# Performance work log

Hardware: AMD Instinct MI355X
Metric: run time of the kernel (lower is better)

Reference implementation:

```python
import jax, jax.numpy as jnp
import numpy as np

H = 100          # hidden size (hard-coded in module)
B, C, T = 256, 9, 1024
NC = 6           # num_classes


def _lstm_layer(xs, W_ih, W_hh, b, h0, c0):
    """xs: [B,T,In] -> hidden sequence [B,T,H]. Torch gate order i,f,g,o."""
    # Precompute the input projection for all timesteps in one big GEMM.
    pre = jnp.einsum('bti,gi->btg', xs, W_ih) + b   # [B,T,4H]
    pre_t = jnp.swapaxes(pre, 0, 1)                 # [T,B,4H]

    def step(carry, p):
        h, c = carry
        g = p + h @ W_hh.T                          # [B,4H]
        i, f, gg, o = jnp.split(g, 4, axis=-1)
        c = jax.nn.sigmoid(f) * c + jax.nn.sigmoid(i) * jnp.tanh(gg)
        h = jax.nn.sigmoid(o) * jnp.tanh(c)
        return (h, c), h

    (_, _), hs = jax.lax.scan(step, (h0, c0), pre_t)
    return jnp.swapaxes(hs, 0, 1)                   # [B,T,H]


def setup_inputs() -> dict:
    key = jax.random.key(0)
    ks = jax.random.split(key, 14)
    s = 0.1  # ~ uniform(-1/sqrt(H), 1/sqrt(H)) scale of torch default init
    n = lambda k, shape, sc=s: jax.random.normal(k, shape, dtype=jnp.float32) * sc
    return {
        'x':     jax.random.normal(ks[0], (B, C, T), dtype=jnp.float32),
        'h0_1':  jax.random.normal(ks[1], (B, H), dtype=jnp.float32),
        'c0_1':  jax.random.normal(ks[2], (B, H), dtype=jnp.float32),
        'h0_2':  jax.random.normal(ks[3], (B, H), dtype=jnp.float32),
        'c0_2':  jax.random.normal(ks[4], (B, H), dtype=jnp.float32),
        'W_ih1': n(ks[5], (4 * H, C)),
        'W_hh1': n(ks[6], (4 * H, H)),
        'b1':    n(ks[7], (4 * H,)),   # b_ih + b_hh folded together
        'W_ih2': n(ks[8], (4 * H, H)),
        'W_hh2': n(ks[9], (4 * H, H)),
        'b2':    n(ks[10], (4 * H,)),
        'W_fc':  n(ks[11], (NC, H)),
        'b_fc':  n(ks[12], (NC,)),
    }


def reference(x, h0_1, c0_1, h0_2, c0_2, W_ih1, W_hh1, b1,
              W_ih2, W_hh2, b2, W_fc, b_fc):
    xs = jnp.swapaxes(x, 1, 2)                      # [B,T,C] (x.transpose(1,2))
    h1 = _lstm_layer(xs, W_ih1, W_hh1, b1, h0_1, c0_1)   # [B,T,H]
    h2 = _lstm_layer(h1, W_ih2, W_hh2, b2, h0_2, c0_2)   # [B,T,H]
    out = h2[:, -1, :] @ W_fc.T + b_fc              # [B,NC]
    return out
```

## Files before the change

### kernel.cpp

```cpp
#include <hip/hip_runtime.h>

#define HH   100
#define G4   400
#define BB   256
#define CC   9
#define TT   1024
#define NCLS 6
#define XSTR 13
#define CH   64
#define NCH  (TT/CH)
#define TSTR 128

__device__ __forceinline__ float sigm(float x) {
    return __fdividef(1.0f, 1.0f + __expf(-x));
}
__device__ __forceinline__ float tanh_fast(float x) {
    return 2.0f * sigm(2.0f * x) - 1.0f;
}
__device__ __forceinline__ float bcast(float v, int l) {
    return __int_as_float(__builtin_amdgcn_readlane(__float_as_int(v), l));
}

__global__ __launch_bounds__(512, 2)
void lstm_layer1(const float* __restrict__ x,
                 const float* __restrict__ h0,
                 const float* __restrict__ c0,
                 const float* __restrict__ W_ih,
                 const float* __restrict__ W_hh,
                 const float* __restrict__ bias_g,
                 float* __restrict__ h1out)
{
    const int b    = blockIdx.x;
    const int tid  = threadIdx.x;
    const int lane = tid & 63;

    __shared__ float xT[TT * XSTR + 64];
    __shared__ float hb[128];
    __shared__ float gates[448];

    const float* xb = x + (size_t)b * CC * TT;
    for (int i = tid; i < CC * TT; i += 512) {
        int c  = i >> 10;
        int tp = i & 1023;
        xT[tp * XSTR + c] = xb[i];
    }
    if (tid < 128) hb[tid] = (tid < HH) ? h0[b * HH + tid] : 0.0f;
    float c_reg = (tid < HH) ? c0[b * HH + tid] : 0.0f;

    const bool comp = (tid < 448);
    const int  row  = (tid < G4) ? tid : 0;

    float w[CC + HH], bg = 0.0f;
    if (comp) {
        #pragma unroll
        for (int j = 0; j < CC; ++j) w[j] = W_ih[row * CC + j];
        #pragma unroll
        for (int j = 0; j < HH; ++j) w[CC + j] = W_hh[row * HH + j];
        bg = bias_g[row];
        #pragma unroll
        for (int j = 0; j < CC + HH; ++j) asm volatile("" : "+v"(w[j]));
    }
    const bool isG = (row >= 2 * HH && row < 3 * HH);
    float* hout = h1out + (size_t)b * TT * HH;
    __syncthreads();

    #pragma unroll 1
    for (int t = 0; t < TT; ++t) {
        if (comp) {
            float vx = xT[t * XSTR + lane];
            float va = hb[lane];
            float vb = hb[64 + lane];
            asm volatile("" : "+v"(vx), "+v"(va), "+v"(vb));
            float a0 = bg, a1 = 0.f;
            #pragma unroll
            for (int c = 0; c < CC; ++c) {
                float h_ = bcast(vx, c);
                if (c & 1) a1 += h_ * w[c]; else a0 += h_ * w[c];
            }
            #pragma unroll
            for (int j = 0; j < 64; ++j) {
                float h_ = bcast(va, j);
                if (j & 1) a1 += h_ * w[CC + j]; else a0 += h_ * w[CC + j];
            }
            #pragma unroll
            for (int j = 0; j < 36; ++j) {
                float h_ = bcast(vb, j);
                if (j & 1) a1 += h_ * w[CC + 64 + j]; else a0 += h_ * w[CC + 64 + j];
            }
            gates[tid] = a0 + a1;
        }
        __syncthreads();
        if (tid < HH) {
            float ri = gates[tid];
            float rf = gates[tid + HH];
            float rg = gates[tid + 2 * HH];
            float ro = gates[tid + 3 * HH];
            float cc = sigm(rf) * c_reg + sigm(ri) * tanh_fast(rg);
            c_reg = cc;
            float hv = sigm(ro) * tanh_fast(cc);
            hb[tid] = hv;
            hout[t * HH + tid] = hv;
        }
        __syncthreads();
    }
    (void)isG;
}

__global__ __launch_bounds__(512, 2)
void lstm_layer2_fc(const float* __restrict__ h1,
                    const float* __restrict__ h0,
                    const float* __restrict__ c0,
                    const float* __restrict__ W_ih,
                    const float* __restrict__ W_hh,
                    const float* __restrict__ bias_g,
                    const float* __restrict__ W_fc,
                    const float* __restrict__ b_fc,
                    float* __restrict__ out)
{
    const int b    = blockIdx.x;
    const int tid  = threadIdx.x;
    const int lane = tid & 63;

    __shared__ float tile[CH * TSTR];
    __shared__ float preS[CH * G4];
    __shared__ float hb[128];

    if (tid < 128) hb[tid] = (tid < HH) ? h0[b * HH + tid] : 0.0f;
    float c_reg = (tid < HH) ? c0[b * HH + tid] : 0.0f;

    const bool comp = (tid < 448);
    const int  row  = (tid < G4) ? tid : 0;
    const float bg  = comp ? bias_g[row] : 0.0f;

    const float* h1b = h1 + (size_t)b * TT * HH;
    __syncthreads();

    #pragma unroll 1
    for (int ch = 0; ch < NCH; ++ch) {
        const int t0 = ch * CH;
        for (int i = tid; i < CH * 25; i += 512) {
            int r = i / 25;
            int c = i - r * 25;
            ((float4*)(tile + r * TSTR))[c] =
                ((const float4*)(h1b + (size_t)(t0 + r) * HH))[c];
        }
        __syncthreads();

        {
            const float* wsrc = W_ih + (size_t)row * HH;
            asm volatile("" : "+v"(wsrc));
            if (comp) {
                float wv[HH];
                #pragma unroll
                for (int j = 0; j < HH / 4; ++j)
                    *(float4*)&wv[4 * j] = ((const float4*)wsrc)[j];
                #pragma unroll
                for (int j = 0; j < HH; ++j) asm volatile("" : "+v"(wv[j]));
                #pragma unroll 1
                for (int t = 0; t < CH; ++t) {
                    float va = tile[t * TSTR + lane];
                    float vb = tile[t * TSTR + 64 + lane];
                    asm volatile("" : "+v"(va), "+v"(vb));
                    float a0 = bg, a1 = 0.f;
                    #pragma unroll
                    for (int j = 0; j < 64; ++j) {
                        float h_ = bcast(va, j);
                        if (j & 1) a1 += h_ * wv[j]; else a0 += h_ * wv[j];
                    }
                    #pragma unroll
                    for (int j = 0; j < 36; ++j) {
                        float h_ = bcast(vb, j);
                        if (j & 1) a1 += h_ * wv[64 + j]; else a0 += h_ * wv[64 + j];
                    }
                    if (tid < G4) preS[t * G4 + row] = a0 + a1;
                }
            }
        }
        __syncthreads();

        {
            const float* wsrc = W_hh + (size_t)row * HH;
            asm volatile("" : "+v"(wsrc));
            float wv[HH];
            if (comp) {
                #pragma unroll
                for (int j = 0; j < HH / 4; ++j)
                    *(float4*)&wv[4 * j] = ((const float4*)wsrc)[j];
                #pragma unroll
                for (int j = 0; j < HH; ++j) asm volatile("" : "+v"(wv[j]));
            }
            #pragma unroll 1
            for (int t = 0; t < CH; ++t) {
                if (comp) {
                    float va = hb[lane];
                    float vb = hb[64 + lane];
                    asm volatile("" : "+v"(va), "+v"(vb));
                    float a0 = 0.f, a1 = 0.f;
                    #pragma unroll
                    for (int j = 0; j < 64; ++j) {
                        float h_ = bcast(va, j);
                        if (j & 1) a1 += h_ * wv[j]; else a0 += h_ * wv[j];
                    }
                    #pragma unroll
                    for (int j = 0; j < 36; ++j) {
                        float h_ = bcast(vb, j);
                        if (j & 1) a1 += h_ * wv[64 + j]; else a0 += h_ * wv[64 + j];
                    }
                    if (tid < G4) preS[t * G4 + row] += a0 + a1;
                }
                __syncthreads();
                if (tid < HH) {
                    float ri = preS[t * G4 + tid];
                    float rf = preS[t * G4 + HH + tid];
                    float rg = preS[t * G4 + 2 * HH + tid];
                    float ro = preS[t * G4 + 3 * HH + tid];
                    float cc = sigm(rf) * c_reg + sigm(ri) * tanh_fast(rg);
                    c_reg = cc;
                    hb[tid] = sigm(ro) * tanh_fast(cc);
                }
                __syncthreads();
            }
        }
    }

    if (tid < NCLS) {
        float acc = b_fc[tid];
        #pragma unroll 4
        for (int j = 0; j < HH; ++j) acc += W_fc[tid * HH + j] * hb[j];
        out[b * NCLS + tid] = acc;
    }
}

extern "C" void kernel_launch(void* const* d_in, const int* in_sizes, int n_in,
                              void* d_out, int out_size, void* d_ws, size_t ws_size,
                              hipStream_t stream) {
    const float* x     = (const float*)d_in[0];
    const float* h0_1  = (const float*)d_in[1];
    const float* c0_1  = (const float*)d_in[2];
    const float* h0_2  = (const float*)d_in[3];
    const float* c0_2  = (const float*)d_in[4];
    const float* W_ih1 = (const float*)d_in[5];
    const float* W_hh1 = (const float*)d_in[6];
    const float* b1    = (const float*)d_in[7];
    const float* W_ih2 = (const float*)d_in[8];
    const float* W_hh2 = (const float*)d_in[9];
    const float* b2    = (const float*)d_in[10];
    const float* W_fc  = (const float*)d_in[11];
    const float* b_fc  = (const float*)d_in[12];
    float* out = (float*)d_out;

    float* h1 = (float*)d_ws;

    lstm_layer1<<<BB, 512, 0, stream>>>(x, h0_1, c0_1, W_ih1, W_hh1, b1, h1);
    lstm_layer2_fc<<<BB, 512, 0, stream>>>(h1, h0_2, c0_2, W_ih2, W_hh2, b2,
                                           W_fc, b_fc, out);
}
```

Before: 2.926 ms.

## Split input projections into parallel kernels and chunk recurrence across launches

Moves the input-projection GEMMs for both LSTM layers out of the serial recurrence into separate xproj/hproj kernels that run over a 2D grid of batch by time tile. A shared lstm_rec kernel then runs only the h·W_hh recurrence over time chunks, reading precomputed gates from a workspace buffer and carrying h/c state between launches. The goal is to take the parallel input-projection work off the latency-bound sequential path of layer 2. The cost is more kernel launches, extra global-memory traffic for the pre-activation buffer, and a dependence on workspace size for the chunk length.

```diff
diff --git a/kernel.cpp b/kernel.cpp
--- a/kernel.cpp
+++ b/kernel.cpp
@@ -6,10 +6,6 @@
 #define CC   9
 #define TT   1024
 #define NCLS 6
-#define XSTR 13
-#define CH   64
-#define NCH  (TT/CH)
-#define TSTR 128
 
 __device__ __forceinline__ float sigm(float x) {
     return __fdividef(1.0f, 1.0f + __expf(-x));
@@ -20,74 +16,160 @@
 __device__ __forceinline__ float bcast(float v, int l) {
     return __int_as_float(__builtin_amdgcn_readlane(__float_as_int(v), l));
 }
+__device__ __forceinline__ const float* launder(const float* p) {
+    asm volatile("" : "+v"(p));
+    return p;
+}
 
 __global__ __launch_bounds__(512, 2)
-void lstm_layer1(const float* __restrict__ x,
-                 const float* __restrict__ h0,
-                 const float* __restrict__ c0,
-                 const float* __restrict__ W_ih,
-                 const float* __restrict__ W_hh,
-                 const float* __restrict__ bias_g,
-                 float* __restrict__ h1out)
+void xproj(const float* __restrict__ x,
+           const float* __restrict__ W_ih,
+           const float* __restrict__ bias,
+           float* __restrict__ pre,
+           int tbase, int chSteps)
+{
+    const int b    = blockIdx.x;
+    const int tile = blockIdx.y;
+    const int tid  = threadIdx.x;
+    const int t0g  = tbase + tile * 64;
+
+    __shared__ float xt[CC][64];
+    for (int i = tid; i < CC * 64; i += 512) {
+        int c = i >> 6, k = i & 63;
+        xt[c][k] = x[(size_t)b * CC * TT + c * TT + t0g + k];
+    }
+    __syncthreads();
+
+    if (tid < G4) {
+        const float* w = launder(W_ih + tid * CC);
+        float wv[CC];
+        #pragma unroll
+        for (int c = 0; c < CC; ++c) wv[c] = w[c];
+        const float bg = bias[tid];
+        float* po = pre + ((size_t)b * chSteps + tile * 64) * G4 + tid;
+        #pragma unroll 1
+        for (int k = 0; k < 64; ++k) {
+            float a = bg;
+            #pragma unroll
+            for (int c = 0; c < CC; ++c) a += wv[c] * xt[c][k];
+            po[(size_t)k * G4] = a;
+        }
+    }
+}
+
+__global__ __launch_bounds__(512, 2)
+void hproj(const float* __restrict__ h1,
+           const float* __restrict__ W_ih,
+           const float* __restrict__ bias,
+           float* __restrict__ pre,
+           int tbase, int chSteps)
+{
+    const int b    = blockIdx.x;
+    const int tile = blockIdx.y;
+    const int tid  = threadIdx.x;
+    const int lane = tid & 63;
+    const int t0g  = tbase + tile * 64;
+
+    __shared__ float ht[64][128];
+    for (int i = tid; i < 64 * 25; i += 512) {
+        int r = i / 25, c = i - r * 25;
+        *((float4*)&ht[r][4 * c]) =
+            *((const float4*)(h1 + ((size_t)b * TT + t0g + r) * HH) + c);
+    }
+    __syncthreads();
+
+    if (tid < 448) {
+        const int row = (tid < G4) ? tid : 0;
+        const float* w = launder(W_ih + row * HH);
+        float wv[HH];
+        #pragma unroll
+        for (int j = 0; j < HH / 4; ++j)
+            *(float4*)&wv[4 * j] = ((const float4*)w)[j];
+        const float bg = bias[row];
+        float* po = pre + ((size_t)b * chSteps + tile * 64) * G4 + row;
+        #pragma unroll 1
+        for (int k = 0; k < 64; ++k) {
+            float va = ht[k][lane];
+            float vb = ht[k][64 + lane];
+            asm volatile("" : "+v"(va), "+v"(vb));
+            float a0 = bg, a1 = 0.f;
+            #pragma unroll
+            for (int j = 0; j < 64; ++j) {
+                float s = bcast(va, j);
+                if (j & 1) a1 += s * wv[j]; else a0 += s * wv[j];
+            }
+            #pragma unroll
+            for (int j = 0; j < 36; ++j) {
+                float s = bcast(vb, j);
+                if (j & 1) a1 += s * wv[64 + j]; else a0 += s * wv[64 + j];
+            }
+            if (tid < G4) po[(size_t)k * G4] = a0 + a1;
+        }
+    }
+}
+
+__global__ __launch_bounds__(512, 2)
+void lstm_rec(const float* __restrict__ pre,
+              const float* __restrict__ h0,
+              const float* __restrict__ c0,
+              const float* __restrict__ W_hh,
+              float* __restrict__ h1out,
+              float* __restrict__ st,
+              const float* __restrict__ W_fc,
+              const float* __restrict__ b_fc,
+              float* __restrict__ out,
+              int tbase, int chSteps, int flags)
 {
     const int b    = blockIdx.x;
     const int tid  = threadIdx.x;
     const int lane = tid & 63;
-
-    __shared__ float xT[TT * XSTR + 64];
+    const bool first = (tbase == 0);
+
     __shared__ float hb[128];
     __shared__ float gates[448];
 
-    const float* xb = x + (size_t)b * CC * TT;
-    for (int i = tid; i < CC * TT; i += 512) {
-        int c  = i >> 10;
-        int tp = i & 1023;
-        xT[tp * XSTR + c] = xb[i];
-    }
-    if (tid < 128) hb[tid] = (tid < HH) ? h0[b * HH + tid] : 0.0f;
-    float c_reg = (tid < HH) ? c0[b * HH + tid] : 0.0f;
+    if (tid < 128)
+        hb[tid] = (tid < HH)
+                    ? (first ? h0[b * HH + tid] : st[b * 200 + tid])
+                    : 0.0f;
+    float c_reg = (tid < HH)
+                    ? (first ? c0[b * HH + tid] : st[b * 200 + HH + tid])
+                    : 0.0f;
 
     const bool comp = (tid < 448);
     const int  row  = (tid < G4) ? tid : 0;
-
-    float w[CC + HH], bg = 0.0f;
+    float wv[HH];
     if (comp) {
+        const float* w = launder(W_hh + row * HH);
         #pragma unroll
-        for (int j = 0; j < CC; ++j) w[j] = W_ih[row * CC + j];
-        #pragma unroll
-        for (int j = 0; j < HH; ++j) w[CC + j] = W_hh[row * HH + j];
-        bg = bias_g[row];
-        #pragma unroll
-        for (int j = 0; j < CC + HH; ++j) asm volatile("" : "+v"(w[j]));
-    }
-    const bool isG = (row >= 2 * HH && row < 3 * HH);
-    float* hout = h1out + (size_t)b * TT * HH;
+        for (int j = 0; j < HH / 4; ++j)
+            *(float4*)&wv[4 * j] = ((const float4*)w)[j];
+    }
+    const float* pb = pre + (size_t)b * chSteps * G4;
+    float preg = comp ? pb[row] : 0.0f;
+    float* hout = (flags & 1) ? (h1out + ((size_t)b * TT + tbase) * HH) : nullptr;
     __syncthreads();
 
     #pragma unroll 1
-    for (int t = 0; t < TT; ++t) {
+    for (int t = 0; t < chSteps; ++t) {
         if (comp) {
-            float vx = xT[t * XSTR + lane];
+            float pnext = (t + 1 < chSteps) ? pb[(size_t)(t + 1) * G4 + row] : 0.f;
             float va = hb[lane];
             float vb = hb[64 + lane];
-            asm volatile("" : "+v"(vx), "+v"(va), "+v"(vb));
-            float a0 = bg, a1 = 0.f;
-            #pragma unroll
-            for (int c = 0; c < CC; ++c) {
-                float h_ = bcast(vx, c);
-                if (c & 1) a1 += h_ * w[c]; else a0 += h_ * w[c];
-            }
+            asm volatile("" : "+v"(va), "+v"(vb));
+            float a0 = preg, a1 = 0.f;
             #pragma unroll
             for (int j = 0; j < 64; ++j) {
-                float h_ = bcast(va, j);
-                if (j & 1) a1 += h_ * w[CC + j]; else a0 += h_ * w[CC + j];
+                float s = bcast(va, j);
+                if (j & 1) a1 += s * wv[j]; else a0 += s * wv[j];
             }
             #pragma unroll
             for (int j = 0; j < 36; ++j) {
-                float h_ = bcast(vb, j);
-                if (j & 1) a1 += h_ * w[CC + 64 + j]; else a0 += h_ * w[CC + 64 + j];
+                float s = bcast(vb, j);
+                if (j & 1) a1 += s * wv[64 + j]; else a0 += s * wv[64 + j];
             }
             gates[tid] = a0 + a1;
+            preg = pnext;
         }
         __syncthreads();
         if (tid < HH) {
@@ -99,131 +181,16 @@
             c_reg = cc;
             float hv = sigm(ro) * tanh_fast(cc);
             hb[tid] = hv;
-            hout[t * HH + tid] = hv;
+            if (flags & 1) hout[(size_t)t * HH + tid] = hv;
         }
         __syncthreads();
     }
-    (void)isG;
-}
-
-__global__ __launch_bounds__(512, 2)
-void lstm_layer2_fc(const float* __restrict__ h1,
-                    const float* __restrict__ h0,
-                    const float* __restrict__ c0,
-                    const float* __restrict__ W_ih,
-                    const float* __restrict__ W_hh,
-                    const float* __restrict__ bias_g,
-                    const float* __restrict__ W_fc,
-                    const float* __restrict__ b_fc,
-                    float* __restrict__ out)
-{
-    const int b    = blockIdx.x;
-    const int tid  = threadIdx.x;
-    const int lane = tid & 63;
-
-    __shared__ float tile[CH * TSTR];
-    __shared__ float preS[CH * G4];
-    __shared__ float hb[128];
-
-    if (tid < 128) hb[tid] = (tid < HH) ? h0[b * HH + tid] : 0.0f;
-    float c_reg = (tid < HH) ? c0[b * HH + tid] : 0.0f;
-
-    const bool comp = (tid < 448);
-    const int  row  = (tid < G4) ? tid : 0;
-    const float bg  = comp ? bias_g[row] : 0.0f;
-
-    const float* h1b = h1 + (size_t)b * TT * HH;
-    __syncthreads();
-
-    #pragma unroll 1
-    for (int ch = 0; ch < NCH; ++ch) {
-        const int t0 = ch * CH;
-        for (int i = tid; i < CH * 25; i += 512) {
-            int r = i / 25;
-            int c = i - r * 25;
-            ((float4*)(tile + r * TSTR))[c] =
-                ((const float4*)(h1b + (size_t)(t0 + r) * HH))[c];
-        }
-        __syncthreads();
-
-        {
-            const float* wsrc = W_ih + (size_t)row * HH;
-            asm volatile("" : "+v"(wsrc));
-            if (comp) {
-                float wv[HH];
-                #pragma unroll
-                for (int j = 0; j < HH / 4; ++j)
-                    *(float4*)&wv[4 * j] = ((const float4*)wsrc)[j];
-                #pragma unroll
-                for (int j = 0; j < HH; ++j) asm volatile("" : "+v"(wv[j]));
-                #pragma unroll 1
-                for (int t = 0; t < CH; ++t) {
-                    float va = tile[t * TSTR + lane];
-                    float vb = tile[t * TSTR + 64 + lane];
-                    asm volatile("" : "+v"(va), "+v"(vb));
-                    float a0 = bg, a1 = 0.f;
-                    #pragma unroll
-                    for (int j = 0; j < 64; ++j) {
-                        float h_ = bcast(va, j);
-                        if (j & 1) a1 += h_ * wv[j]; else a0 += h_ * wv[j];
-                    }
-                    #pragma unroll
-                    for (int j = 0; j < 36; ++j) {
-                        float h_ = bcast(vb, j);
-                        if (j & 1) a1 += h_ * wv[64 + j]; else a0 += h_ * wv[64 + j];
-                    }
-                    if (tid < G4) preS[t * G4 + row] = a0 + a1;
-                }
-            }
-        }
-        __syncthreads();
-
-        {
-            const float* wsrc = W_hh + (size_t)row * HH;
-            asm volatile("" : "+v"(wsrc));
-            float wv[HH];
-            if (comp) {
-                #pragma unroll
-                for (int j = 0; j < HH / 4; ++j)
-                    *(float4*)&wv[4 * j] = ((const float4*)wsrc)[j];
-                #pragma unroll
-                for (int j = 0; j < HH; ++j) asm volatile("" : "+v"(wv[j]));
-            }
-            #pragma unroll 1
-            for (int t = 0; t < CH; ++t) {
-                if (comp) {
-                    float va = hb[lane];
-                    float vb = hb[64 + lane];
-                    asm volatile("" : "+v"(va), "+v"(vb));
-                    float a0 = 0.f, a1 = 0.f;
-                    #pragma unroll
-                    for (int j = 0; j < 64; ++j) {
-                        float h_ = bcast(va, j);
-                        if (j & 1) a1 += h_ * wv[j]; else a0 += h_ * wv[j];
-                    }
-                    #pragma unroll
-                    for (int j = 0; j < 36; ++j) {
-                        float h_ = bcast(vb, j);
-                        if (j & 1) a1 += h_ * wv[64 + j]; else a0 += h_ * wv[64 + j];
-                    }
-                    if (tid < G4) preS[t * G4 + row] += a0 + a1;
-                }
-                __syncthreads();
-                if (tid < HH) {
-                    float ri = preS[t * G4 + tid];
-                    float rf = preS[t * G4 + HH + tid];
-                    float rg = preS[t * G4 + 2 * HH + tid];
-                    float ro = preS[t * G4 + 3 * HH + tid];
-                    float cc = sigm(rf) * c_reg + sigm(ri) * tanh_fast(rg);
-                    c_reg = cc;
-                    hb[tid] = sigm(ro) * tanh_fast(cc);
-                }
-                __syncthreads();
-            }
-        }
-    }
-
-    if (tid < NCLS) {
+
+    if (tid < HH) {
+        st[b * 200 + tid]      = hb[tid];
+        st[b * 200 + HH + tid] = c_reg;
+    }
+    if ((flags & 2) && tid < NCLS) {
         float acc = b_fc[tid];
         #pragma unroll 4
         for (int j = 0; j < HH; ++j) acc += W_fc[tid * HH + j] * hb[j];
@@ -249,9 +216,33 @@
     const float* b_fc  = (const float*)d_in[12];
     float* out = (float*)d_out;
 
-    float* h1 = (float*)d_ws;
-
-    lstm_layer1<<<BB, 512, 0, stream>>>(x, h0_1, c0_1, W_ih1, W_hh1, b1, h1);
-    lstm_layer2_fc<<<BB, 512, 0, stream>>>(h1, h0_2, c0_2, W_ih2, W_hh2, b2,
-                                           W_fc, b_fc, out);
-}
+    char* ws = (char*)d_ws;
+    const size_t h1_bytes = (size_t)BB * TT * HH * 4;
+    const size_t st_bytes = (size_t)BB * 200 * 4;
+    float* h1  = (float*)ws;
+    float* st1 = (float*)(ws + h1_bytes);
+    float* st2 = (float*)(ws + h1_bytes + st_bytes);
+    float* pre = (float*)(ws + h1_bytes + 2 * st_bytes);
+
+    size_t avail = (ws_size > h1_bytes + 2 * st_bytes)
+                     ? ws_size - h1_bytes - 2 * st_bytes : 0;
+    int CH = (int)(avail / ((size_t)BB * G4 * 4));
+    CH = (CH / 64) * 64;
+    if (CH > TT) CH = TT;
+    if (CH < 64) CH = 64;
+    if (CH > 256) CH = 256;
+
+    for (int t0 = 0; t0 < TT; t0 += CH) {
+        int ns = (TT - t0 < CH) ? (TT - t0) : CH;
+        xproj<<<dim3(BB, ns / 64), 512, 0, stream>>>(x, W_ih1, b1, pre, t0, ns);
+        lstm_rec<<<BB, 512, 0, stream>>>(pre, h0_1, c0_1, W_hh1, h1, st1,
+                                         nullptr, nullptr, nullptr, t0, ns, 1);
+    }
+    for (int t0 = 0; t0 < TT; t0 += CH) {
+        int ns = (TT - t0 < CH) ? (TT - t0) : CH;
+        int flags = (t0 + ns >= TT) ? 2 : 0;
+        hproj<<<dim3(BB, ns / 64), 512, 0, stream>>>(h1, W_ih2, b2, pre, t0, ns);
+        lstm_rec<<<BB, 512, 0, stream>>>(pre, h0_2, c0_2, W_hh2, nullptr, st2,
+                                         W_fc, b_fc, out, t0, ns, flags);
+    }
+}
```

Result: no change. 2.929 ms (+0.1%).
